# Performance work log

Measured on AMD Instinct MI355X. Metric: run time of the kernel, lower is better.

The kernel has to match this reference:

```python
import jax, jax.numpy as jnp
import numpy as np

B, T, C = 2, 2048, 1024
H = 16
D = C // H
EPS = 1e-5


def _layernorm(x, g, b):
    mu = jnp.mean(x, axis=-1, keepdims=True)
    var = jnp.mean(jnp.square(x - mu), axis=-1, keepdims=True)
    return (x - mu) * jax.lax.rsqrt(var + EPS) * g + b


def setup_inputs() -> dict:
    key = jax.random.key(0)
    ks = jax.random.split(key, 8)
    s = lambda fan_in: 1.0 / np.sqrt(fan_in)
    return {
        "x": jax.random.normal(ks[0], (B, T, C), dtype=jnp.float32),
        "ln1_g": jnp.ones((C,), jnp.float32),
        "ln1_b": jnp.zeros((C,), jnp.float32),
        "w_qkv": jax.random.uniform(ks[1], (C, 3 * C), jnp.float32, -s(C), s(C)),
        "b_qkv": jnp.zeros((3 * C,), jnp.float32),
        "w_attn_proj": jax.random.uniform(ks[2], (C, C), jnp.float32, -s(C), s(C)),
        "b_attn_proj": jnp.zeros((C,), jnp.float32),
        "ln2_g": jnp.ones((C,), jnp.float32),
        "ln2_b": jnp.zeros((C,), jnp.float32),
        "w_fc": jax.random.uniform(ks[3], (C, 4 * C), jnp.float32, -s(C), s(C)),
        "b_fc": jnp.zeros((4 * C,), jnp.float32),
        "w_out": jax.random.uniform(ks[4], (4 * C, C), jnp.float32, -s(4 * C), s(4 * C)),
        "b_out": jnp.zeros((C,), jnp.float32),
    }


def reference(x, ln1_g, ln1_b, w_qkv, b_qkv, w_attn_proj, b_attn_proj,
              ln2_g, ln2_b, w_fc, b_fc, w_out, b_out):
    # --- masked multi-head attention on ln1(x) ---
    h = _layernorm(x, ln1_g, ln1_b)
    qkv = h @ w_qkv + b_qkv                      # [B,T,3C]
    q, k, v = jnp.split(qkv, 3, axis=-1)
    q = q.reshape(B, T, H, D)
    k = k.reshape(B, T, H, D)
    v = v.reshape(B, T, H, D)
    # NOTE: source scales by emb_dim**-0.5 (not head_dim**-0.5) — kept faithful.
    wei = jnp.einsum('bqhd,bkhd->bhqk', q, k) * (C ** -0.5)
    causal = jnp.tril(jnp.ones((T, T), dtype=bool))
    wei = jnp.where(causal, wei, -jnp.inf)
    attn = jax.nn.softmax(wei, axis=-1)
    out = jnp.einsum('bhqk,bkhd->bqhd', attn, v).reshape(B, T, C)
    x = x + out @ w_attn_proj + b_attn_proj
    # --- GELU MLP on ln2(x) ---
    h = _layernorm(x, ln2_g, ln2_b)
    h = jax.nn.gelu(h @ w_fc + b_fc, approximate=False)
    return x + h @ w_out + b_out
```

## Files before the change

### kernel.cpp

```cpp
#include <hip/hip_runtime.h>
#include <hip/hip_bf16.h>
#include <math.h>

#define BB 2
#define TT 2048
#define CC 1024
#define HH 16
#define DD 64
#define EPS 1e-5f

typedef __bf16 bf16x8 __attribute__((ext_vector_type(8)));
typedef float f32x4 __attribute__((ext_vector_type(4)));

struct alignas(8) bf4 { __bf16 v[4]; };

__device__ __forceinline__ void gld16(const void* g, void* l) {
    __builtin_amdgcn_global_load_lds(
        (const __attribute__((address_space(1))) void*)g,
        (__attribute__((address_space(3))) void*)l, 16, 0, 0);
}

__device__ __forceinline__ f32x4 mfma16(bf16x8 a, bf16x8 b, f32x4 c) {
    return __builtin_amdgcn_mfma_f32_16x16x32_bf16(a, b, c, 0, 0, 0);
}

__global__ __launch_bounds__(256) void wt_cvt_kernel(const float* __restrict__ w,
                                                     __bf16* __restrict__ wt,
                                                     int K, int N) {
    __shared__ float tile[32][33];
    const int tx = threadIdx.x & 31, ty = threadIdx.x >> 5;
    const int k0 = blockIdx.x * 32, n0 = blockIdx.y * 32;
    #pragma unroll
    for (int i = 0; i < 4; ++i)
        tile[ty + i * 8][tx] = w[(size_t)(k0 + ty + i * 8) * N + n0 + tx];
    __syncthreads();
    #pragma unroll
    for (int i = 0; i < 4; ++i)
        wt[(size_t)(n0 + ty + i * 8) * K + k0 + tx] = (__bf16)tile[tx][ty + i * 8];
}

__global__ __launch_bounds__(256) void ln_kernel(const float* __restrict__ x,
                                                 const float* __restrict__ gg,
                                                 const float* __restrict__ bb,
                                                 __bf16* __restrict__ out) {
    __shared__ float red[4];
    __shared__ float red2[4];
    const int row = blockIdx.x;
    const int t = threadIdx.x;
    const float4 v = *(const float4*)(x + (size_t)row * CC + t * 4);

    float s = v.x + v.y + v.z + v.w;
    #pragma unroll
    for (int o = 32; o; o >>= 1) s += __shfl_down(s, o);
    const int lane = t & 63, w = t >> 6;
    if (lane == 0) red[w] = s;
    __syncthreads();
    const float mu = (red[0] + red[1] + red[2] + red[3]) * (1.0f / CC);

    const float dx = v.x - mu, dy = v.y - mu, dz = v.z - mu, dw = v.w - mu;
    float s2 = dx * dx + dy * dy + dz * dz + dw * dw;
    #pragma unroll
    for (int o = 32; o; o >>= 1) s2 += __shfl_down(s2, o);
    if (lane == 0) red2[w] = s2;
    __syncthreads();
    const float var = (red2[0] + red2[1] + red2[2] + red2[3]) * (1.0f / CC);
    const float rstd = rsqrtf(var + EPS);

    const float4 g4 = *(const float4*)(gg + t * 4);
    const float4 b4 = *(const float4*)(bb + t * 4);
    bf4 o4;
    o4.v[0] = (__bf16)(dx * rstd * g4.x + b4.x);
    o4.v[1] = (__bf16)(dy * rstd * g4.y + b4.y);
    o4.v[2] = (__bf16)(dz * rstd * g4.z + b4.z);
    o4.v[3] = (__bf16)(dw * rstd * g4.w + b4.w);
    *(bf4*)(out + (size_t)row * CC + t * 4) = o4;
}

template <int BN, int MODE>
__global__ __launch_bounds__(256) void mfma_gemm(const __bf16* __restrict__ A,
                                                 const __bf16* __restrict__ Bt,
                                                 const float* __restrict__ bias,
                                                 const float* __restrict__ resid,
                                                 void* __restrict__ Cv,
                                                 int M, int N, int K) {
    constexpr int NT = BN / 32;
    __shared__ __bf16 As[128 * 32];
    __shared__ __bf16 Bs[BN * 32];
    const int t = threadIdx.x;
    const int w = t >> 6, lane = t & 63;
    const int quad = lane >> 4, ln = lane & 15;
    const int m0 = blockIdx.y * 128, n0 = blockIdx.x * BN;
    const int wm = (w >> 1) * 64, wn = (w & 1) * (BN / 2);

    f32x4 acc[4][NT];
    #pragma unroll
    for (int im = 0; im < 4; ++im)
        #pragma unroll
        for (int in = 0; in < NT; ++in) acc[im][in] = (f32x4){0.f, 0.f, 0.f, 0.f};

    const int srow = t >> 2;
    const int scol = (((t & 3) ^ ((t >> 3) & 3)) << 3);
    const __bf16* gA = A + (size_t)(m0 + srow) * K + scol;
    const __bf16* gB = Bt + (size_t)(n0 + srow) * K + scol;
    __bf16* lA = &As[t * 8];
    __bf16* lB = &Bs[t * 8];
    const int sw = (ln >> 1) & 3;

    for (int k0 = 0; k0 < K; k0 += 32) {
        __syncthreads();
        gld16(gA + k0, lA);
        gld16(gA + k0 + (size_t)64 * K, lA + 64 * 32);
        gld16(gB + k0, lB);
        if (BN == 128) gld16(gB + k0 + (size_t)64 * K, lB + 64 * 32);
        __syncthreads();

        bf16x8 af[4], bfr[NT];
        #pragma unroll
        for (int im = 0; im < 4; ++im)
            af[im] = *(const bf16x8*)&As[(wm + im * 16 + ln) * 32 + ((quad ^ sw) << 3)];
        #pragma unroll
        for (int in = 0; in < NT; ++in)
            bfr[in] = *(const bf16x8*)&Bs[(wn + in * 16 + ln) * 32 + ((quad ^ sw) << 3)];
        #pragma unroll
        for (int im = 0; im < 4; ++im)
            #pragma unroll
            for (int in = 0; in < NT; ++in)
                acc[im][in] = mfma16(af[im], bfr[in], acc[im][in]);
    }

    #pragma unroll
    for (int in = 0; in < NT; ++in) {
        const int col = n0 + wn + in * 16 + ln;
        const float bv = bias[col];
        #pragma unroll
        for (int im = 0; im < 4; ++im) {
            const int row = m0 + wm + im * 16 + (quad << 2);
            if (MODE == 4) {
                bf4 pk;
                #pragma unroll
                for (int r = 0; r < 4; ++r) pk.v[r] = (__bf16)(acc[im][in][r] + bv);
                __bf16* dst = (__bf16*)Cv +
                    ((size_t)(((row >> 11) * HH + (col >> 6)) * DD + (col & 63))) * TT +
                    (row & 2047);
                *(bf4*)dst = pk;
            } else {
                #pragma unroll
                for (int r = 0; r < 4; ++r) {
                    float v = acc[im][in][r] + bv;
                    const size_t off = (size_t)(row + r) * N + col;
                    if (MODE == 2) {
                        v = 0.5f * v * (1.0f + erff(v * 0.70710678118654752f));
                        ((__bf16*)Cv)[off] = (__bf16)v;
                    } else if (MODE == 3) {
                        ((__bf16*)Cv)[off] = (__bf16)v;
                    } else if (MODE == 1) {
                        ((float*)Cv)[off] = v + resid[off];
                    } else {
                        ((float*)Cv)[off] = v;
                    }
                }
            }
        }
    }
}

#define PSTR 72

__global__ __launch_bounds__(256) void flash_mfma_kernel(
    const __bf16* __restrict__ qk,
    const __bf16* __restrict__ vT,
    __bf16* __restrict__ out) {
    __shared__ __bf16 Ks[2][64 * 64];
    __shared__ __bf16 Vs[2][64 * 64];
    __shared__ __bf16 Ps[4][16 * PSTR];

    const int px = blockIdx.x;
    const int h = blockIdx.y, b = blockIdx.z;
    const int t = threadIdx.x;
    const int w = t >> 6, lane = t & 63;
    const int quad = lane >> 4, ln = lane & 15;
    const float scale = 0.03125f;

    const int pc0 = t, pc1 = t + 256;
    const int rr0 = pc0 >> 3, c0 = (pc0 & 7) ^ (rr0 & 7);
    const int rr1 = pc1 >> 3, c1 = (pc1 & 7) ^ (rr1 & 7);
    const __bf16* gK0 = qk + (size_t)(b * TT + rr0) * (2 * CC) + CC + h * DD + c0 * 8;
    const __bf16* gK1 = qk + (size_t)(b * TT + rr1) * (2 * CC) + CC + h * DD + c1 * 8;
    const __bf16* gV0 = vT + ((size_t)((b * HH + h) * DD) + rr0) * TT + c0 * 8;
    const __bf16* gV1 = vT + ((size_t)((b * HH + h) * DD) + rr1) * TT + c1 * 8;

    #pragma unroll
    for (int phase = 0; phase < 2; ++phase) {
        const int qt = phase ? px : (31 - px);

        const size_t qrow = (size_t)(b * TT + qt * 64 + w * 16 + ln);
        const bf16x8 qf0 = *(const bf16x8*)&qk[qrow * (2 * CC) + h * DD + quad * 8];
        const bf16x8 qf1 = *(const bf16x8*)&qk[qrow * (2 * CC) + h * DD + 32 + quad * 8];

        f32x4 oacc[4];
        #pragma unroll
        for (int nd = 0; nd < 4; ++nd) oacc[nd] = (f32x4){0.f, 0.f, 0.f, 0.f};
        f32x4 lacc = (f32x4){0.f, 0.f, 0.f, 0.f};

        __syncthreads();
        gld16(gK0, &Ks[0][pc0 * 8]);
        gld16(gK1, &Ks[0][pc1 * 8]);
        gld16(gV0, &Vs[0][pc0 * 8]);
        gld16(gV1, &Vs[0][pc1 * 8]);

        int cur = 0;
        for (int kt = 0; kt <= qt; ++kt) {
            __syncthreads();
            if (kt < qt) {
                const int nx = cur ^ 1;
                const size_t ko = (size_t)(kt + 1) * 64 * (2 * CC);
                const int vo = (kt + 1) * 64;
                gld16(gK0 + ko, &Ks[nx][pc0 * 8]);
                gld16(gK1 + ko, &Ks[nx][pc1 * 8]);
                gld16(gV0 + vo, &Vs[nx][pc0 * 8]);
                gld16(gV1 + vo, &Vs[nx][pc1 * 8]);
            }

            const int ntmax = (kt == qt) ? w : 3;

            f32x4 p[4];
            #pragma unroll
            for (int nt = 0; nt < 4; ++nt) {
                if (nt <= ntmax) {
                    const bf16x8 kf0 = *(const bf16x8*)
                        &Ks[cur][(nt * 16 + ln) * 64 + ((quad ^ (ln & 7)) << 3)];
                    const bf16x8 kf1 = *(const bf16x8*)
                        &Ks[cur][(nt * 16 + ln) * 64 + (((4 + quad) ^ (ln & 7)) << 3)];
                    f32x4 z = (f32x4){0.f, 0.f, 0.f, 0.f};
                    z = mfma16(qf0, kf0, z);
                    z = mfma16(qf1, kf1, z);
                    #pragma unroll
                    for (int r = 0; r < 4; ++r) {
                        float pv = __expf(z[r] * scale);
                        if (kt == qt && nt == ntmax && ln > quad * 4 + r) pv = 0.f;
                        p[nt][r] = pv;
                    }
                } else {
                    p[nt] = (f32x4){0.f, 0.f, 0.f, 0.f};
                }
            }

            #pragma unroll
            for (int r = 0; r < 4; ++r)
                lacc[r] += (p[0][r] + p[1][r]) + (p[2][r] + p[3][r]);

            #pragma unroll
            for (int nt = 0; nt < 4; ++nt)
                #pragma unroll
                for (int r = 0; r < 4; ++r)
                    Ps[w][(quad * 4 + r) * PSTR + nt * 16 + ln] = (__bf16)p[nt][r];

            const bf16x8 pf0 = *(const bf16x8*)&Ps[w][ln * PSTR + quad * 8];
            const bf16x8 pf1 = *(const bf16x8*)&Ps[w][ln * PSTR + 32 + quad * 8];
            #pragma unroll
            for (int nd = 0; nd < 4; ++nd) {
                const bf16x8 vf0 = *(const bf16x8*)
                    &Vs[cur][(nd * 16 + ln) * 64 + ((quad ^ (ln & 7)) << 3)];
                const bf16x8 vf1 = *(const bf16x8*)
                    &Vs[cur][(nd * 16 + ln) * 64 + (((4 + quad) ^ (ln & 7)) << 3)];
                oacc[nd] = mfma16(pf0, vf0, oacc[nd]);
                oacc[nd] = mfma16(pf1, vf1, oacc[nd]);
            }
            cur ^= 1;
        }

        float lr[4];
        #pragma unroll
        for (int r = 0; r < 4; ++r) {
            lr[r] = lacc[r];
            #pragma unroll
            for (int off = 1; off < 16; off <<= 1)
                lr[r] += __shfl_xor(lr[r], off);
        }

        #pragma unroll
        for (int r = 0; r < 4; ++r) {
            const float inv = 1.0f / lr[r];
            const size_t orow = (size_t)(b * TT + qt * 64 + w * 16 + quad * 4 + r);
            #pragma unroll
            for (int nd = 0; nd < 4; ++nd)
                out[orow * CC + h * DD + nd * 16 + ln] = (__bf16)(oacc[nd][r] * inv);
        }
    }
}

extern "C" void kernel_launch(void* const* d_in, const int* in_sizes, int n_in,
                              void* d_out, int out_size, void* d_ws, size_t ws_size,
                              hipStream_t stream) {
    const float* x       = (const float*)d_in[0];
    const float* ln1_g   = (const float*)d_in[1];
    const float* ln1_b   = (const float*)d_in[2];
    const float* w_qkv   = (const float*)d_in[3];
    const float* b_qkv   = (const float*)d_in[4];
    const float* w_proj  = (const float*)d_in[5];
    const float* b_proj  = (const float*)d_in[6];
    const float* ln2_g   = (const float*)d_in[7];
    const float* ln2_b   = (const float*)d_in[8];
    const float* w_fc    = (const float*)d_in[9];
    const float* b_fc    = (const float*)d_in[10];
    const float* w_out   = (const float*)d_in[11];
    const float* b_out   = (const float*)d_in[12];
    float* out = (float*)d_out;

    char* ws = (char*)d_ws;
    const size_t MB = 1024ull * 1024ull;
    __bf16* h_bf   = (__bf16*)(ws + 0);
    __bf16* wqkvT  = (__bf16*)(ws + 8 * MB);
    __bf16* wprojT = (__bf16*)(ws + 14 * MB);
    __bf16* wfcT   = (__bf16*)(ws + 16 * MB);
    __bf16* woutT  = (__bf16*)(ws + 24 * MB);
    __bf16* qk_bf  = (__bf16*)(ws + 32 * MB);
    __bf16* vT     = (__bf16*)(ws + 48 * MB);
    __bf16* attn   = (__bf16*)(ws + 56 * MB);
    float*  x2     = (float*)(ws + 64 * MB);
    __bf16* fc_out = (__bf16*)(ws + 32 * MB);

    const int M = BB * TT;

    wt_cvt_kernel<<<dim3(32, 96), 256, 0, stream>>>(w_qkv, wqkvT, CC, 3 * CC);
    wt_cvt_kernel<<<dim3(32, 32), 256, 0, stream>>>(w_proj, wprojT, CC, CC);
    wt_cvt_kernel<<<dim3(32, 128), 256, 0, stream>>>(w_fc, wfcT, CC, 4 * CC);
    wt_cvt_kernel<<<dim3(128, 32), 256, 0, stream>>>(w_out, woutT, 4 * CC, CC);

    ln_kernel<<<M, 256, 0, stream>>>(x, ln1_g, ln1_b, h_bf);
    mfma_gemm<128, 3><<<dim3(2 * CC / 128, M / 128), 256, 0, stream>>>(
        h_bf, wqkvT, b_qkv, nullptr, qk_bf, M, 2 * CC, CC);
    mfma_gemm<128, 4><<<dim3(CC / 128, M / 128), 256, 0, stream>>>(
        h_bf, wqkvT + (size_t)(2 * CC) * CC, b_qkv + 2 * CC, nullptr, vT, M, CC, CC);
    flash_mfma_kernel<<<dim3(TT / 128, HH, BB), 256, 0, stream>>>(qk_bf, vT, attn);
    mfma_gemm<64, 1><<<dim3(CC / 64, M / 128), 256, 0, stream>>>(
        attn, wprojT, b_proj, x, x2, M, CC, CC);
    ln_kernel<<<M, 256, 0, stream>>>(x2, ln2_g, ln2_b, h_bf);
    mfma_gemm<128, 2><<<dim3(4 * CC / 128, M / 128), 256, 0, stream>>>(
        h_bf, wfcT, b_fc, nullptr, fc_out, M, 4 * CC, CC);
    mfma_gemm<64, 1><<<dim3(CC / 64, M / 128), 256, 0, stream>>>(
        fc_out, woutT, b_out, x2, out, M, CC, 4 * CC);
}
```

Baseline: 412.0 us.

## Double GEMM K-tile to 64 and fuse QK and V projections into one launch

The GEMM now stages a 64-wide K slice per barrier pair instead of 32, using an 8-way XOR swizzle and two MFMA half-steps per tile. This halves the number of syncthreads and loop iterations. The separate QK and V projection launches are merged into one MODE 5 kernel whose epilogue writes either row-major QK or transposed V depending on the column block. Shared memory per block doubles, which may reduce occupancy.

```diff
diff --git a/kernel.cpp b/kernel.cpp
--- a/kernel.cpp
+++ b/kernel.cpp
@@ -82,10 +82,11 @@
                                                  const float* __restrict__ bias,
                                                  const float* __restrict__ resid,
                                                  void* __restrict__ Cv,
+                                                 void* __restrict__ Cv2,
                                                  int M, int N, int K) {
     constexpr int NT = BN / 32;
-    __shared__ __bf16 As[128 * 32];
-    __shared__ __bf16 Bs[BN * 32];
+    __shared__ __bf16 As[128 * 64];
+    __shared__ __bf16 Bs[BN * 64];
     const int t = threadIdx.x;
     const int w = t >> 6, lane = t & 63;
     const int quad = lane >> 4, ln = lane & 15;
@@ -98,34 +99,40 @@
         #pragma unroll
         for (int in = 0; in < NT; ++in) acc[im][in] = (f32x4){0.f, 0.f, 0.f, 0.f};
 
-    const int srow = t >> 2;
-    const int scol = (((t & 3) ^ ((t >> 3) & 3)) << 3);
+    const int srow = t >> 3;
+    const int scol = ((t & 7) ^ (srow & 7)) << 3;
     const __bf16* gA = A + (size_t)(m0 + srow) * K + scol;
     const __bf16* gB = Bt + (size_t)(n0 + srow) * K + scol;
     __bf16* lA = &As[t * 8];
     __bf16* lB = &Bs[t * 8];
-    const int sw = (ln >> 1) & 3;
-
-    for (int k0 = 0; k0 < K; k0 += 32) {
+
+    for (int k0 = 0; k0 < K; k0 += 64) {
         __syncthreads();
-        gld16(gA + k0, lA);
-        gld16(gA + k0 + (size_t)64 * K, lA + 64 * 32);
-        gld16(gB + k0, lB);
-        if (BN == 128) gld16(gB + k0 + (size_t)64 * K, lB + 64 * 32);
+        #pragma unroll
+        for (int j = 0; j < 4; ++j)
+            gld16(gA + k0 + (size_t)(j * 32) * K, lA + j * 2048);
+        #pragma unroll
+        for (int j = 0; j < BN / 32; ++j)
+            gld16(gB + k0 + (size_t)(j * 32) * K, lB + j * 2048);
         __syncthreads();
 
-        bf16x8 af[4], bfr[NT];
-        #pragma unroll
-        for (int im = 0; im < 4; ++im)
-            af[im] = *(const bf16x8*)&As[(wm + im * 16 + ln) * 32 + ((quad ^ sw) << 3)];
-        #pragma unroll
-        for (int in = 0; in < NT; ++in)
-            bfr[in] = *(const bf16x8*)&Bs[(wn + in * 16 + ln) * 32 + ((quad ^ sw) << 3)];
-        #pragma unroll
-        for (int im = 0; im < 4; ++im)
+        #pragma unroll
+        for (int half = 0; half < 2; ++half) {
+            bf16x8 af[4], bfr[NT];
+            #pragma unroll
+            for (int im = 0; im < 4; ++im)
+                af[im] = *(const bf16x8*)&As[(wm + im * 16 + ln) * 64 +
+                                             (((half * 4 + quad) ^ (ln & 7)) << 3)];
             #pragma unroll
             for (int in = 0; in < NT; ++in)
-                acc[im][in] = mfma16(af[im], bfr[in], acc[im][in]);
+                bfr[in] = *(const bf16x8*)&Bs[(wn + in * 16 + ln) * 64 +
+                                              (((half * 4 + quad) ^ (ln & 7)) << 3)];
+            #pragma unroll
+            for (int im = 0; im < 4; ++im)
+                #pragma unroll
+                for (int in = 0; in < NT; ++in)
+                    acc[im][in] = mfma16(af[im], bfr[in], acc[im][in]);
+        }
     }
 
     #pragma unroll
@@ -135,14 +142,22 @@
         #pragma unroll
         for (int im = 0; im < 4; ++im) {
             const int row = m0 + wm + im * 16 + (quad << 2);
-            if (MODE == 4) {
-                bf4 pk;
-                #pragma unroll
-                for (int r = 0; r < 4; ++r) pk.v[r] = (__bf16)(acc[im][in][r] + bv);
-                __bf16* dst = (__bf16*)Cv +
-                    ((size_t)(((row >> 11) * HH + (col >> 6)) * DD + (col & 63))) * TT +
-                    (row & 2047);
-                *(bf4*)dst = pk;
+            if (MODE == 5) {
+                if (n0 + wn + in * 16 < 2 * CC) {
+                    #pragma unroll
+                    for (int r = 0; r < 4; ++r)
+                        ((__bf16*)Cv)[(size_t)(row + r) * (2 * CC) + col] =
+                            (__bf16)(acc[im][in][r] + bv);
+                } else {
+                    const int cv = col - 2 * CC;
+                    bf4 pk;
+                    #pragma unroll
+                    for (int r = 0; r < 4; ++r) pk.v[r] = (__bf16)(acc[im][in][r] + bv);
+                    __bf16* dst = (__bf16*)Cv2 +
+                        ((size_t)(((row >> 11) * HH + (cv >> 6)) * DD + (cv & 63))) * TT +
+                        (row & 2047);
+                    *(bf4*)dst = pk;
+                }
             } else {
                 #pragma unroll
                 for (int r = 0; r < 4; ++r) {
@@ -151,12 +166,8 @@
                     if (MODE == 2) {
                         v = 0.5f * v * (1.0f + erff(v * 0.70710678118654752f));
                         ((__bf16*)Cv)[off] = (__bf16)v;
-                    } else if (MODE == 3) {
-                        ((__bf16*)Cv)[off] = (__bf16)v;
                     } else if (MODE == 1) {
                         ((float*)Cv)[off] = v + resid[off];
-                    } else {
-                        ((float*)Cv)[off] = v;
                     }
                 }
             }
@@ -328,16 +339,14 @@
     wt_cvt_kernel<<<dim3(128, 32), 256, 0, stream>>>(w_out, woutT, 4 * CC, CC);
 
     ln_kernel<<<M, 256, 0, stream>>>(x, ln1_g, ln1_b, h_bf);
-    mfma_gemm<128, 3><<<dim3(2 * CC / 128, M / 128), 256, 0, stream>>>(
-        h_bf, wqkvT, b_qkv, nullptr, qk_bf, M, 2 * CC, CC);
-    mfma_gemm<128, 4><<<dim3(CC / 128, M / 128), 256, 0, stream>>>(
-        h_bf, wqkvT + (size_t)(2 * CC) * CC, b_qkv + 2 * CC, nullptr, vT, M, CC, CC);
+    mfma_gemm<128, 5><<<dim3(3 * CC / 128, M / 128), 256, 0, stream>>>(
+        h_bf, wqkvT, b_qkv, nullptr, qk_bf, vT, M, 3 * CC, CC);
     flash_mfma_kernel<<<dim3(TT / 128, HH, BB), 256, 0, stream>>>(qk_bf, vT, attn);
     mfma_gemm<64, 1><<<dim3(CC / 64, M / 128), 256, 0, stream>>>(
-        attn, wprojT, b_proj, x, x2, M, CC, CC);
+        attn, wprojT, b_proj, x, x2, nullptr, M, CC, CC);
     ln_kernel<<<M, 256, 0, stream>>>(x2, ln2_g, ln2_b, h_bf);
     mfma_gemm<128, 2><<<dim3(4 * CC / 128, M / 128), 256, 0, stream>>>(
-        h_bf, wfcT, b_fc, nullptr, fc_out, M, 4 * CC, CC);
+        h_bf, wfcT, b_fc, nullptr, fc_out, nullptr, M, 4 * CC, CC);
     mfma_gemm<64, 1><<<dim3(CC / 64, M / 128), 256, 0, stream>>>(
-        fc_out, woutT, b_out, x2, out, M, CC, 4 * CC);
-}
+        fc_out, woutT, b_out, x2, out, nullptr, M, CC, 4 * CC);
+}
```

New measurement: 363.0 us. 11.9% less time.
